# Performance work log

Measured on AMD Instinct MI355X. Metric: run time of the kernel, lower is better.

The kernel has to match this reference:

```python
import jax, jax.numpy as jnp
import numpy as np

N_EXPERTS = 8
TOP_K = 2


def setup_inputs() -> dict:
    key = jax.random.key(0)
    k1, k2, k3, k4 = jax.random.split(key, 4)
    B, S, D, E = 8, 4096, 1024, N_EXPERTS
    x = jax.random.normal(k1, (B, S, D), dtype=jnp.float32)
    gate_w = jax.random.normal(k2, (D, E), dtype=jnp.float32) * (1.0 / np.sqrt(D))
    expert_w = jax.random.normal(k3, (E, D, D), dtype=jnp.float32) * (1.0 / np.sqrt(D))
    expert_b = jax.random.normal(k4, (E, D), dtype=jnp.float32) * 0.01
    return {"x": x, "gate_w": gate_w, "expert_w": expert_w, "expert_b": expert_b}


def reference(x, gate_w, expert_w, expert_b):
    B, S, D = x.shape
    E = expert_w.shape[0]
    xt = x.reshape(-1, D)                       # [T, D], T = B*S
    T = xt.shape[0]
    gate_logits = xt @ gate_w                   # [T, E]
    weights, selected = jax.lax.top_k(gate_logits, TOP_K)   # [T, K]
    weights = jax.nn.softmax(weights.astype(jnp.float32), axis=1).astype(x.dtype)
    # Per-token combine weights over experts (top-k indices are distinct -> scatter-add is exact)
    combine = jnp.zeros((T, E), dtype=x.dtype).at[jnp.arange(T)[:, None], selected].add(weights)  # [T, E]
    out = jnp.zeros_like(xt)
    for e in range(E):  # fixed small expert count, mirrors the module's expert loop
        out = out + combine[:, e:e + 1] * (xt @ expert_w[e] + expert_b[e])
    return out.reshape(x.shape)
```

## Files before the change

### kernel.cpp

```cpp
#include <hip/hip_runtime.h>
#include <hip/hip_bf16.h>


typedef __attribute__((ext_vector_type(8))) short short8_t;
typedef __attribute__((ext_vector_type(4))) float f32x4_t;

#define GLOAD_LDS16(g, l)                                                                     \
  __builtin_amdgcn_global_load_lds((const __attribute__((address_space(1))) unsigned int*)(g), \
                                   (__attribute__((address_space(3))) unsigned int*)(l), 16, 0, 0)

__device__ __forceinline__ unsigned short f2bf(float f) {
  union { __hip_bfloat16 h; unsigned short u; } c;
  c.h = __float2bfloat16(f);
  return c.u;
}

__global__ __launch_bounds__(256) void gate_kernel(
    const float* __restrict__ x, const float* __restrict__ gw,
    unsigned short* __restrict__ xb,
    int* __restrict__ tok_e, float* __restrict__ tok_w)
{
  int wid = threadIdx.x >> 6, lane = threadIdx.x & 63;
  int t0 = (blockIdx.x << 4) + (wid << 2);
  const float4* g4 = (const float4*)gw;
  float lg[4][8] = {};
  #pragma unroll
  for (int c = 0; c < 4; ++c) {
    int d4 = (c << 6) + lane;
    float4 ga[4], gb[4];
    #pragma unroll
    for (int j = 0; j < 4; ++j) {
      int d = (d4 << 2) + j;
      ga[j] = g4[d << 1];
      gb[j] = g4[(d << 1) + 1];
    }
    #pragma unroll
    for (int t = 0; t < 4; ++t) {
      const float4* x4 = (const float4*)(x + ((size_t)(t0 + t) << 10));
      float4 v = x4[d4];
      unsigned long long pk = (unsigned long long)f2bf(v.x)
                            | ((unsigned long long)f2bf(v.y) << 16)
                            | ((unsigned long long)f2bf(v.z) << 32)
                            | ((unsigned long long)f2bf(v.w) << 48);
      ((unsigned long long*)(xb + ((size_t)(t0 + t) << 10)))[d4] = pk;
      float xs[4] = {v.x, v.y, v.z, v.w};
      #pragma unroll
      for (int j = 0; j < 4; ++j) {
        lg[t][0] += xs[j]*ga[j].x; lg[t][1] += xs[j]*ga[j].y;
        lg[t][2] += xs[j]*ga[j].z; lg[t][3] += xs[j]*ga[j].w;
        lg[t][4] += xs[j]*gb[j].x; lg[t][5] += xs[j]*gb[j].y;
        lg[t][6] += xs[j]*gb[j].z; lg[t][7] += xs[j]*gb[j].w;
      }
    }
  }
  #pragma unroll
  for (int t = 0; t < 4; ++t)
    #pragma unroll
    for (int e = 0; e < 8; ++e) {
      float v = lg[t][e];
      #pragma unroll
      for (int s = 32; s > 0; s >>= 1) v += __shfl_xor(v, s, 64);
      lg[t][e] = v;
    }
  if (lane < 4) {
    int t = t0 + lane;
    float m0 = lg[lane][0], m1 = -3.4e38f; int e0 = 0, e1 = 0;
    #pragma unroll
    for (int e = 1; e < 8; ++e) {
      float v = lg[lane][e];
      if (v > m0) { m1 = m0; e1 = e0; m0 = v; e0 = e; }
      else if (v > m1) { m1 = v; e1 = e; }
    }
    float p1 = 1.0f / (1.0f + expf(m0 - m1));
    float p0 = 1.0f - p1;
    int i0 = t << 1;
    tok_e[i0]   = e0; tok_w[i0]   = p0;
    tok_e[i0+1] = e1; tok_w[i0+1] = p1;
  }
}

__global__ __launch_bounds__(256) void hist_kernel(
    const int* __restrict__ tok_e, int* __restrict__ tok_r, int* __restrict__ chunkhist)
{
  __shared__ int lh[8];
  if (threadIdx.x < 8) lh[threadIdx.x] = 0;
  __syncthreads();
  int i = (blockIdx.x << 8) + threadIdx.x;
  int e = tok_e[i];
  tok_r[i] = atomicAdd(&lh[e], 1);
  __syncthreads();
  if (threadIdx.x < 8) chunkhist[(blockIdx.x << 3) + threadIdx.x] = lh[threadIdx.x];
}

__global__ __launch_bounds__(512) void scan_kernel(
    const int* __restrict__ chunkhist, int* __restrict__ base, int* __restrict__ ctrl)
{
  __shared__ int h[2048];
  __shared__ int bx[2048];
  __shared__ int tot[8], eoff[8];
  for (int i = threadIdx.x; i < 2048; i += 512) h[i] = chunkhist[i];
  __syncthreads();
  int wid = threadIdx.x >> 6, lane = threadIdx.x & 63;
  int running = 0;
  #pragma unroll
  for (int b = 0; b < 4; ++b) {
    int c = (b << 6) + lane;
    int orig = h[(c << 3) + wid];
    int v = orig;
    #pragma unroll
    for (int s = 1; s < 64; s <<= 1) {
      int u = __shfl_up(v, s, 64);
      if (lane >= s) v += u;
    }
    bx[(c << 3) + wid] = running + v - orig;
    running += __shfl(v, 63, 64);
  }
  if (lane == 0) tot[wid] = running;
  __syncthreads();
  if (threadIdx.x == 0) {
    int off = 0, boff = 0;
    #pragma unroll
    for (int e = 0; e < 8; ++e) {
      ctrl[e] = tot[e];
      ctrl[8 + e] = off; eoff[e] = off; off += tot[e];
      ctrl[16 + e] = boff; boff += (tot[e] + 127) >> 7;
    }
    ctrl[24] = boff;
  }
  __syncthreads();
  for (int i = threadIdx.x; i < 2048; i += 512) base[i] = bx[i] + eoff[i & 7];
}

__global__ __launch_bounds__(256) void scatter_kernel(
    const int* __restrict__ tok_e, const int* __restrict__ tok_r, const float* __restrict__ tok_w,
    const int* __restrict__ base, int* __restrict__ slot_token, float* __restrict__ slot_w,
    int* __restrict__ tok_slot)
{
  int i = (blockIdx.x << 8) + threadIdx.x;
  int e = tok_e[i];
  int slot = base[((i >> 8) << 3) + e] + tok_r[i];
  slot_token[slot] = i >> 1;
  slot_w[slot] = tok_w[i];
  tok_slot[i] = slot;
}

__global__ __launch_bounds__(256) void wconv_kernel(const float* __restrict__ w,
                                                    unsigned short* __restrict__ wt)
{
  __shared__ float tile[32][33];
  const float* we = w + ((size_t)blockIdx.z << 20);
  unsigned short* wte = wt + ((size_t)blockIdx.z << 20);
  int k0 = blockIdx.x << 5, n0 = blockIdx.y << 5;
  for (int i = threadIdx.x; i < 1024; i += 256) {
    int k = i >> 5, n = i & 31;
    tile[k][n] = we[(size_t)(k0 + k) * 1024 + n0 + n];
  }
  __syncthreads();
  for (int i = threadIdx.x; i < 1024; i += 256) {
    int n = i >> 5, k = i & 31;
    wte[(size_t)(n0 + n) * 1024 + k0 + k] = f2bf(tile[k][n]);
  }
}

__global__ __launch_bounds__(256, 3) void moe_gemm(
    const unsigned short* __restrict__ xb, const unsigned short* __restrict__ wt,
    const float* __restrict__ bias, const int* __restrict__ ctrl,
    const int* __restrict__ slot_token, const float* __restrict__ slot_w,
    float* __restrict__ ybuf, float* __restrict__ out, int total_slots, int use_ybuf)
{
  __shared__ unsigned short Alds[3 * 128 * 32];
  __shared__ unsigned short Blds[3 * 128 * 32];
  __shared__ int   tokid[128];
  __shared__ float wrow[128];

  int d = blockIdx.x;
  int s_ = d >> 3, xcd = d & 7;
  int by = ((s_ >> 3) << 3) | xcd;
  int bx = s_ & 7;
  if (by >= ctrl[24]) return;
  int e = 0;
  #pragma unroll
  for (int i = 1; i < 8; ++i) if (by >= ctrl[16 + i]) e = i;
  int mblk = by - ctrl[16 + e];
  int cnt  = ctrl[e];
  int slot0 = ctrl[8 + e] + (mblk << 7);
  int rows_valid = cnt - (mblk << 7); if (rows_valid > 128) rows_valid = 128;

  int tid = threadIdx.x;
  if (tid < 128) {
    int s = slot0 + tid; if (s > total_slots - 1) s = total_slots - 1;
    tokid[tid] = slot_token[s];
    wrow[tid]  = slot_w[s];
  }
  __syncthreads();

  int lane = tid & 63, w = tid >> 6;
  int wr = w >> 1, wc = w & 1;
  int l15 = lane & 15, hk = lane >> 4;
  int bn0 = bx << 7;
  const unsigned short* wte = wt + ((size_t)e << 20);

  int c0 = tid, c1 = tid + 256;
  int r0 = c0 >> 2, k0 = (c0 & 3) ^ ((r0 >> 1) & 3);
  int r1 = c1 >> 2, k1 = (c1 & 3) ^ ((r1 >> 1) & 3);
  const unsigned short* gA0 = xb + ((size_t)tokid[r0] << 10) + (k0 << 3);
  const unsigned short* gA1 = xb + ((size_t)tokid[r1] << 10) + (k1 << 3);
  const unsigned short* gB0 = wte + ((size_t)(bn0 + r0) << 10) + (k0 << 3);
  const unsigned short* gB1 = wte + ((size_t)(bn0 + r1) << 10) + (k1 << 3);
  int lo0 = (w << 6) << 3;
  int lo1 = ((w << 6) + 256) << 3;

  f32x4_t acc[4][4] = {};

#define STAGE(NB, KO)                                                         \
  GLOAD_LDS16(gA0 + (KO), &Alds[(NB) * 4096 + lo0]);                          \
  GLOAD_LDS16(gA1 + (KO), &Alds[(NB) * 4096 + lo1]);                          \
  GLOAD_LDS16(gB0 + (KO), &Blds[(NB) * 4096 + lo0]);                          \
  GLOAD_LDS16(gB1 + (KO), &Blds[(NB) * 4096 + lo1]);

#define COMPUTE(BUF)                                                          \
  { short8_t aF[4], bF[4];                                                    \
    _Pragma("unroll") for (int m = 0; m < 4; ++m) {                           \
      int ar = (wr << 6) + (m << 4) + l15;                                    \
      aF[m] = *(const short8_t*)&Alds[(BUF) * 4096 + (ar << 5) + ((hk ^ ((ar >> 1) & 3)) << 3)]; } \
    _Pragma("unroll") for (int n = 0; n < 4; ++n) {                           \
      int br = (wc << 6) + (n << 4) + l15;                                    \
      bF[n] = *(const short8_t*)&Blds[(BUF) * 4096 + (br << 5) + ((hk ^ ((br >> 1) & 3)) << 3)]; } \
    __builtin_amdgcn_s_setprio(1);                                            \
    _Pragma("unroll") for (int m = 0; m < 4; ++m)                             \
    _Pragma("unroll") for (int n = 0; n < 4; ++n)                             \
      acc[m][n] = __builtin_amdgcn_mfma_f32_16x16x32_bf16(aF[m], bF[n], acc[m][n], 0, 0, 0); \
    __builtin_amdgcn_s_setprio(0); }

#define VM4 asm volatile("s_waitcnt vmcnt(4)" ::: "memory");
#define BARR __builtin_amdgcn_s_barrier();

  STAGE(0, 0)
  STAGE(1, 32)
  VM4
  BARR
  for (int i = 0; i < 10; ++i) {
    int t = i * 3;
    STAGE(2, (t + 2) << 5)
    COMPUTE(0)
    VM4
    BARR
    STAGE(0, (t + 3) << 5)
    COMPUTE(1)
    VM4
    BARR
    STAGE(1, (t + 4) << 5)
    COMPUTE(2)
    VM4
    BARR
  }
  COMPUTE(0)
  asm volatile("s_waitcnt vmcnt(0)" ::: "memory");
  BARR
  COMPUTE(1)
#undef STAGE
#undef COMPUTE
#undef VM4
#undef BARR

  const float* be = bias + (e << 10);
  float bv[4];
  #pragma unroll
  for (int nf = 0; nf < 4; ++nf) bv[nf] = be[bn0 + (wc << 6) + (nf << 4) + l15];
  #pragma unroll
  for (int mf = 0; mf < 4; ++mf) {
    int rbase = (wr << 6) + (mf << 4) + (hk << 2);
    #pragma unroll
    for (int r = 0; r < 4; ++r) {
      int row = rbase + r;
      if (row < rows_valid) {
        float wv = wrow[row];
        if (use_ybuf) {
          size_t obase = ((size_t)(slot0 + row) << 10);
          #pragma unroll
          for (int nf = 0; nf < 4; ++nf) {
            int dout = bn0 + (wc << 6) + (nf << 4) + l15;
            ybuf[obase + dout] = wv * (acc[mf][nf][r] + bv[nf]);
          }
        } else {
          size_t obase = ((size_t)tokid[row] << 10);
          #pragma unroll
          for (int nf = 0; nf < 4; ++nf) {
            int dout = bn0 + (wc << 6) + (nf << 4) + l15;
            atomicAdd(&out[obase + dout], wv * (acc[mf][nf][r] + bv[nf]));
          }
        }
      }
    }
  }
}

__global__ __launch_bounds__(256) void combine_kernel(
    const float* __restrict__ ybuf, const int* __restrict__ tok_slot, float* __restrict__ out)
{
  int t = blockIdx.x;
  int s0 = tok_slot[t << 1], s1 = tok_slot[(t << 1) + 1];
  const float4* y0 = (const float4*)(ybuf + ((size_t)s0 << 10));
  const float4* y1 = (const float4*)(ybuf + ((size_t)s1 << 10));
  float4 a = y0[threadIdx.x], b = y1[threadIdx.x];
  float4 r; r.x = a.x + b.x; r.y = a.y + b.y; r.z = a.z + b.z; r.w = a.w + b.w;
  ((float4*)(out + ((size_t)t << 10)))[threadIdx.x] = r;
}

extern "C" void kernel_launch(void* const* d_in, const int* in_sizes, int n_in,
                              void* d_out, int out_size, void* d_ws, size_t ws_size,
                              hipStream_t stream) {
  (void)n_in;
  const float* x  = (const float*)d_in[0];
  const float* gw = (const float*)d_in[1];
  const float* ew = (const float*)d_in[2];
  const float* eb = (const float*)d_in[3];
  int T  = in_sizes[0] >> 10;
  int T2 = T << 1;

  char* wsb = (char*)d_ws;
  unsigned short* xb = (unsigned short*)wsb;
  size_t off = (size_t)T * 1024 * 2;
  unsigned short* wt = (unsigned short*)(wsb + off);
  off += (size_t)8 * 1024 * 1024 * 2;
  int* ctrl = (int*)(wsb + off); off += 256;
  int* tok_e = (int*)(wsb + off); off += (size_t)T2 * 4;
  int* tok_r = (int*)(wsb + off); off += (size_t)T2 * 4;
  float* tok_w = (float*)(wsb + off); off += (size_t)T2 * 4;
  int* slot_token = (int*)(wsb + off); off += (size_t)T2 * 4;
  float* slot_w = (float*)(wsb + off); off += (size_t)T2 * 4;
  int* tok_slot = (int*)(wsb + off); off += (size_t)T2 * 4;
  int* chunkhist = (int*)(wsb + off); off += 2048 * 4;
  int* base = (int*)(wsb + off); off += 2048 * 4;
  float* ybuf = (float*)(wsb + off);
  size_t need = off + (size_t)T2 * 1024 * 4;
  int use_ybuf = (ws_size >= need) ? 1 : 0;

  float* out = (float*)d_out;

  if (!use_ybuf)
    hipMemsetAsync(d_out, 0, (size_t)out_size * sizeof(float), stream);
  gate_kernel<<<T / 16, 256, 0, stream>>>(x, gw, xb, tok_e, tok_w);
  wconv_kernel<<<dim3(32, 32, 8), 256, 0, stream>>>(ew, wt);
  hist_kernel<<<T2 / 256, 256, 0, stream>>>(tok_e, tok_r, chunkhist);
  scan_kernel<<<1, 512, 0, stream>>>(chunkhist, base, ctrl);
  scatter_kernel<<<T2 / 256, 256, 0, stream>>>(tok_e, tok_r, tok_w, base,
                                               slot_token, slot_w, tok_slot);
  moe_gemm<<<4160, 256, 0, stream>>>(xb, wt, eb, ctrl, slot_token, slot_w,
                                     ybuf, out, T2, use_ybuf);
  if (use_ybuf)
    combine_kernel<<<T, 256, 0, stream>>>(ybuf, tok_slot, out);
}
```

Baseline: 365.1 us.

## Enlarge MoE GEMM tiles to 256x256 with 8 waves and phased pipelining

The grouped expert GEMM moves from 128x128 tiles with 4 waves and a triple-buffered K=32 pipeline to 256x256 tiles with 8 waves (2x4 layout), K=64 steps split into two halves, and double buffering. Loads and compute are interleaved in four phases per step, with finer-grained barriers and waitcnts. Expert blocks are now padded to 256 rows, and the grid shrinks to 1056 blocks. The goal is more arithmetic per byte loaded into LDS and fewer global loads. The costs are more padding waste per expert, larger LDS and register use that lowers occupancy, and fewer blocks to spread across CUs.

```diff
diff --git a/kernel.cpp b/kernel.cpp
--- a/kernel.cpp
+++ b/kernel.cpp
@@ -123,7 +123,7 @@
     for (int e = 0; e < 8; ++e) {
       ctrl[e] = tot[e];
       ctrl[8 + e] = off; eoff[e] = off; off += tot[e];
-      ctrl[16 + e] = boff; boff += (tot[e] + 127) >> 7;
+      ctrl[16 + e] = boff; boff += (tot[e] + 255) >> 8;
     }
     ctrl[24] = boff;
   }
@@ -162,32 +162,31 @@
   }
 }
 
-__global__ __launch_bounds__(256, 3) void moe_gemm(
+__global__ __launch_bounds__(512, 2) void moe_gemm(
     const unsigned short* __restrict__ xb, const unsigned short* __restrict__ wt,
     const float* __restrict__ bias, const int* __restrict__ ctrl,
     const int* __restrict__ slot_token, const float* __restrict__ slot_w,
     float* __restrict__ ybuf, float* __restrict__ out, int total_slots, int use_ybuf)
 {
-  __shared__ unsigned short Alds[3 * 128 * 32];
-  __shared__ unsigned short Blds[3 * 128 * 32];
-  __shared__ int   tokid[128];
-  __shared__ float wrow[128];
+  __shared__ unsigned short Alds[2 * 2 * 256 * 32];
+  __shared__ unsigned short Blds[2 * 2 * 256 * 32];
+  __shared__ int   tokid[256];
+  __shared__ float wrow[256];
 
   int d = blockIdx.x;
-  int s_ = d >> 3, xcd = d & 7;
-  int by = ((s_ >> 3) << 3) | xcd;
-  int bx = s_ & 7;
+  int xcd = d & 7, nb = (d >> 3) & 3, gbase = d >> 5;
+  int by = (gbase << 3) | xcd;
   if (by >= ctrl[24]) return;
   int e = 0;
   #pragma unroll
   for (int i = 1; i < 8; ++i) if (by >= ctrl[16 + i]) e = i;
   int mblk = by - ctrl[16 + e];
   int cnt  = ctrl[e];
-  int slot0 = ctrl[8 + e] + (mblk << 7);
-  int rows_valid = cnt - (mblk << 7); if (rows_valid > 128) rows_valid = 128;
+  int slot0 = ctrl[8 + e] + (mblk << 8);
+  int rows_valid = cnt - (mblk << 8); if (rows_valid > 256) rows_valid = 256;
 
   int tid = threadIdx.x;
-  if (tid < 128) {
+  if (tid < 256) {
     int s = slot0 + tid; if (s > total_slots - 1) s = total_slots - 1;
     tokid[tid] = slot_token[s];
     wrow[tid]  = slot_w[s];
@@ -195,81 +194,99 @@
   __syncthreads();
 
   int lane = tid & 63, w = tid >> 6;
-  int wr = w >> 1, wc = w & 1;
+  int wm = w >> 2, wn = w & 3;
   int l15 = lane & 15, hk = lane >> 4;
-  int bn0 = bx << 7;
+  int bn0 = nb << 8;
   const unsigned short* wte = wt + ((size_t)e << 20);
 
-  int c0 = tid, c1 = tid + 256;
-  int r0 = c0 >> 2, k0 = (c0 & 3) ^ ((r0 >> 1) & 3);
-  int r1 = c1 >> 2, k1 = (c1 & 3) ^ ((r1 >> 1) & 3);
-  const unsigned short* gA0 = xb + ((size_t)tokid[r0] << 10) + (k0 << 3);
-  const unsigned short* gA1 = xb + ((size_t)tokid[r1] << 10) + (k1 << 3);
-  const unsigned short* gB0 = wte + ((size_t)(bn0 + r0) << 10) + (k0 << 3);
-  const unsigned short* gB1 = wte + ((size_t)(bn0 + r1) << 10) + (k1 << 3);
-  int lo0 = (w << 6) << 3;
-  int lo1 = ((w << 6) + 256) << 3;
-
-  f32x4_t acc[4][4] = {};
-
-#define STAGE(NB, KO)                                                         \
-  GLOAD_LDS16(gA0 + (KO), &Alds[(NB) * 4096 + lo0]);                          \
-  GLOAD_LDS16(gA1 + (KO), &Alds[(NB) * 4096 + lo1]);                          \
-  GLOAD_LDS16(gB0 + (KO), &Blds[(NB) * 4096 + lo0]);                          \
-  GLOAD_LDS16(gB1 + (KO), &Blds[(NB) * 4096 + lo1]);
-
-#define COMPUTE(BUF)                                                          \
-  { short8_t aF[4], bF[4];                                                    \
-    _Pragma("unroll") for (int m = 0; m < 4; ++m) {                           \
-      int ar = (wr << 6) + (m << 4) + l15;                                    \
-      aF[m] = *(const short8_t*)&Alds[(BUF) * 4096 + (ar << 5) + ((hk ^ ((ar >> 1) & 3)) << 3)]; } \
-    _Pragma("unroll") for (int n = 0; n < 4; ++n) {                           \
-      int br = (wc << 6) + (n << 4) + l15;                                    \
-      bF[n] = *(const short8_t*)&Blds[(BUF) * 4096 + (br << 5) + ((hk ^ ((br >> 1) & 3)) << 3)]; } \
-    __builtin_amdgcn_s_setprio(1);                                            \
-    _Pragma("unroll") for (int m = 0; m < 4; ++m)                             \
-    _Pragma("unroll") for (int n = 0; n < 4; ++n)                             \
-      acc[m][n] = __builtin_amdgcn_mfma_f32_16x16x32_bf16(aF[m], bF[n], acc[m][n], 0, 0, 0); \
-    __builtin_amdgcn_s_setprio(0); }
-
-#define VM4 asm volatile("s_waitcnt vmcnt(4)" ::: "memory");
+  int rr = tid >> 2;
+  int kswz = (tid & 3) ^ ((tid >> 3) & 3);
+  const unsigned short* gA0 = xb + ((size_t)tokid[rr] << 10) + (kswz << 3);
+  const unsigned short* gA1 = xb + ((size_t)tokid[128 + rr] << 10) + (kswz << 3);
+  const unsigned short* gB0 = wte + ((size_t)(bn0 + rr) << 10) + (kswz << 3);
+  const unsigned short* gB1 = wte + ((size_t)(bn0 + 128 + rr) << 10) + (kswz << 3);
+
+  f32x4_t acc[8][4] = {};
+  short8_t aF[8], bFa[2], bFb[2];
+
+#define STG_A(BUF, KH, T)                                                               \
+  GLOAD_LDS16(gA0 + ((T) << 6) + ((KH) << 5), &Alds[(BUF) + ((KH) << 13) + (w << 9)]);  \
+  GLOAD_LDS16(gA1 + ((T) << 6) + ((KH) << 5), &Alds[(BUF) + ((KH) << 13) + 4096 + (w << 9)]);
+#define STG_B(BUF, KH, T)                                                               \
+  GLOAD_LDS16(gB0 + ((T) << 6) + ((KH) << 5), &Blds[(BUF) + ((KH) << 13) + (w << 9)]);  \
+  GLOAD_LDS16(gB1 + ((T) << 6) + ((KH) << 5), &Blds[(BUF) + ((KH) << 13) + 4096 + (w << 9)]);
+
+#define RD_AF(BUF, KH)                                                                  \
+  _Pragma("unroll") for (int mf = 0; mf < 8; ++mf) {                                    \
+    int ar = (wm << 7) + (mf << 4) + l15;                                               \
+    aF[mf] = *(const short8_t*)&Alds[(BUF) + ((KH) << 13) + (ar << 5) + ((hk ^ ((ar >> 1) & 3)) << 3)]; }
+#define RD_BF(DST, BUF, KH, NH)                                                         \
+  _Pragma("unroll") for (int i = 0; i < 2; ++i) {                                       \
+    int br = (wn << 6) + ((((NH) << 1) + i) << 4) + l15;                                \
+    DST[i] = *(const short8_t*)&Blds[(BUF) + ((KH) << 13) + (br << 5) + ((hk ^ ((br >> 1) & 3)) << 3)]; }
+
+#define MM(NH, BF)                                                                      \
+  __builtin_amdgcn_s_setprio(1);                                                        \
+  _Pragma("unroll") for (int mf = 0; mf < 8; ++mf)                                      \
+  _Pragma("unroll") for (int i = 0; i < 2; ++i)                                         \
+    acc[mf][((NH) << 1) + i] = __builtin_amdgcn_mfma_f32_16x16x32_bf16(                 \
+        aF[mf], BF[i], acc[mf][((NH) << 1) + i], 0, 0, 0);                              \
+  __builtin_amdgcn_s_setprio(0);
+
+#define PH_SYNC                                                                         \
+  __builtin_amdgcn_s_barrier();                                                         \
+  asm volatile("s_waitcnt lgkmcnt(0)" ::: "memory");                                    \
+  __builtin_amdgcn_sched_barrier(0);
 #define BARR __builtin_amdgcn_s_barrier();
 
-  STAGE(0, 0)
-  STAGE(1, 32)
-  VM4
+  STG_A(0, 0, 0) STG_B(0, 0, 0) STG_A(0, 1, 0) STG_B(0, 1, 0)
+  asm volatile("s_waitcnt vmcnt(4)" ::: "memory");
+  STG_A(16384, 0, 1) STG_B(16384, 0, 1) STG_A(16384, 1, 1)
+  asm volatile("s_waitcnt vmcnt(6)" ::: "memory");
   BARR
-  for (int i = 0; i < 10; ++i) {
-    int t = i * 3;
-    STAGE(2, (t + 2) << 5)
-    COMPUTE(0)
-    VM4
+
+  int cur = 0;
+  for (int t = 0; t < 16; ++t) {
+    int nxt = cur ^ 16384;
+    RD_AF(cur, 0) RD_BF(bFa, cur, 0, 0)
+    if (t < 15) { STG_B(nxt, 1, t + 1) }
+    PH_SYNC
+    MM(0, bFa)
     BARR
-    STAGE(0, (t + 3) << 5)
-    COMPUTE(1)
-    VM4
+    RD_BF(bFb, cur, 0, 1)
+    if (t < 14) { STG_A(cur, 0, t + 2) }
+    PH_SYNC
+    MM(1, bFb)
     BARR
-    STAGE(1, (t + 4) << 5)
-    COMPUTE(2)
-    VM4
+    RD_AF(cur, 1) RD_BF(bFa, cur, 1, 0)
+    if (t < 14) { STG_B(cur, 0, t + 2) }
+    PH_SYNC
+    MM(0, bFa)
     BARR
-  }
-  COMPUTE(0)
-  asm volatile("s_waitcnt vmcnt(0)" ::: "memory");
-  BARR
-  COMPUTE(1)
-#undef STAGE
-#undef COMPUTE
-#undef VM4
+    RD_BF(bFb, cur, 1, 1)
+    if (t < 14) { STG_A(cur, 1, t + 2) }
+    if (t < 14) { asm volatile("s_waitcnt vmcnt(6)" ::: "memory"); }
+    else if (t == 14) { asm volatile("s_waitcnt vmcnt(0)" ::: "memory"); }
+    PH_SYNC
+    MM(1, bFb)
+    BARR
+    cur = nxt;
+  }
+#undef STG_A
+#undef STG_B
+#undef RD_AF
+#undef RD_BF
+#undef MM
+#undef PH_SYNC
 #undef BARR
 
   const float* be = bias + (e << 10);
   float bv[4];
   #pragma unroll
-  for (int nf = 0; nf < 4; ++nf) bv[nf] = be[bn0 + (wc << 6) + (nf << 4) + l15];
-  #pragma unroll
-  for (int mf = 0; mf < 4; ++mf) {
-    int rbase = (wr << 6) + (mf << 4) + (hk << 2);
+  for (int nf = 0; nf < 4; ++nf) bv[nf] = be[bn0 + (wn << 6) + (nf << 4) + l15];
+  #pragma unroll
+  for (int mf = 0; mf < 8; ++mf) {
+    int rbase = (wm << 7) + (mf << 4) + (hk << 2);
     #pragma unroll
     for (int r = 0; r < 4; ++r) {
       int row = rbase + r;
@@ -279,14 +296,14 @@
           size_t obase = ((size_t)(slot0 + row) << 10);
           #pragma unroll
           for (int nf = 0; nf < 4; ++nf) {
-            int dout = bn0 + (wc << 6) + (nf << 4) + l15;
+            int dout = bn0 + (wn << 6) + (nf << 4) + l15;
             ybuf[obase + dout] = wv * (acc[mf][nf][r] + bv[nf]);
           }
         } else {
           size_t obase = ((size_t)tokid[row] << 10);
           #pragma unroll
           for (int nf = 0; nf < 4; ++nf) {
-            int dout = bn0 + (wc << 6) + (nf << 4) + l15;
+            int dout = bn0 + (wn << 6) + (nf << 4) + l15;
             atomicAdd(&out[obase + dout], wv * (acc[mf][nf][r] + bv[nf]));
           }
         }
@@ -346,7 +363,7 @@
   scan_kernel<<<1, 512, 0, stream>>>(chunkhist, base, ctrl);
   scatter_kernel<<<T2 / 256, 256, 0, stream>>>(tok_e, tok_r, tok_w, base,
                                                slot_token, slot_w, tok_slot);
-  moe_gemm<<<4160, 256, 0, stream>>>(xb, wt, eb, ctrl, slot_token, slot_w,
+  moe_gemm<<<1056, 512, 0, stream>>>(xb, wt, eb, ctrl, slot_token, slot_w,
                                      ybuf, out, T2, use_ybuf);
   if (use_ybuf)
     combine_kernel<<<T, 256, 0, stream>>>(ybuf, tok_slot, out);
```

After: 423.5 us. 16.0% more time.

## Widen MoE GEMM tile to 128x256 and store bf16 partials indexed by token

Applied to the files above, without the earlier changes.

The grouped expert GEMM tile grows from 128x128 to 128x256. Each wave now holds a 4x8 MFMA accumulator block, the B staging buffer doubles, and the grid is halved, which raises arithmetic intensity and cuts how often the gathered A rows are reloaded. Per-slot partial outputs are written in bf16 to a buffer indexed by token and k-slot rather than by slot, so the combine kernel no longer needs the tok_slot indirection and moves half the bytes. The costs are lower occupancy (launch bounds 2 instead of 3), higher register pressure, and extra rounding of the partial sums to bf16.

```diff
diff --git a/kernel.cpp b/kernel.cpp
--- a/kernel.cpp
+++ b/kernel.cpp
@@ -4,6 +4,7 @@
 
 typedef __attribute__((ext_vector_type(8))) short short8_t;
 typedef __attribute__((ext_vector_type(4))) float f32x4_t;
+typedef __attribute__((ext_vector_type(4))) unsigned short us4_t;
 
 #define GLOAD_LDS16(g, l)                                                                     \
   __builtin_amdgcn_global_load_lds((const __attribute__((address_space(1))) unsigned int*)(g), \
@@ -13,6 +14,11 @@
   union { __hip_bfloat16 h; unsigned short u; } c;
   c.h = __float2bfloat16(f);
   return c.u;
+}
+__device__ __forceinline__ float bf2f(unsigned short u) {
+  union { unsigned int i; float f; } c;
+  c.i = ((unsigned int)u) << 16;
+  return c.f;
 }
 
 __global__ __launch_bounds__(256) void gate_kernel(
@@ -133,15 +139,13 @@
 
 __global__ __launch_bounds__(256) void scatter_kernel(
     const int* __restrict__ tok_e, const int* __restrict__ tok_r, const float* __restrict__ tok_w,
-    const int* __restrict__ base, int* __restrict__ slot_token, float* __restrict__ slot_w,
-    int* __restrict__ tok_slot)
+    const int* __restrict__ base, int* __restrict__ slot_token, float* __restrict__ slot_w)
 {
   int i = (blockIdx.x << 8) + threadIdx.x;
   int e = tok_e[i];
   int slot = base[((i >> 8) << 3) + e] + tok_r[i];
-  slot_token[slot] = i >> 1;
+  slot_token[slot] = (i >> 1) | ((i & 1) << 16);
   slot_w[slot] = tok_w[i];
-  tok_slot[i] = slot;
 }
 
 __global__ __launch_bounds__(256) void wconv_kernel(const float* __restrict__ w,
@@ -162,21 +166,21 @@
   }
 }
 
-__global__ __launch_bounds__(256, 3) void moe_gemm(
+__global__ __launch_bounds__(256, 2) void moe_gemm(
     const unsigned short* __restrict__ xb, const unsigned short* __restrict__ wt,
     const float* __restrict__ bias, const int* __restrict__ ctrl,
     const int* __restrict__ slot_token, const float* __restrict__ slot_w,
-    float* __restrict__ ybuf, float* __restrict__ out, int total_slots, int use_ybuf)
+    unsigned short* __restrict__ part, float* __restrict__ out, int total_slots, int use_part)
 {
   __shared__ unsigned short Alds[3 * 128 * 32];
-  __shared__ unsigned short Blds[3 * 128 * 32];
+  __shared__ unsigned short Blds[3 * 256 * 32];
   __shared__ int   tokid[128];
+  __shared__ int   kslot[128];
   __shared__ float wrow[128];
 
   int d = blockIdx.x;
-  int s_ = d >> 3, xcd = d & 7;
-  int by = ((s_ >> 3) << 3) | xcd;
-  int bx = s_ & 7;
+  int xcd = d & 7, nb = (d >> 3) & 3, gbase = d >> 5;
+  int by = (gbase << 3) | xcd;
   if (by >= ctrl[24]) return;
   int e = 0;
   #pragma unroll
@@ -189,69 +193,73 @@
   int tid = threadIdx.x;
   if (tid < 128) {
     int s = slot0 + tid; if (s > total_slots - 1) s = total_slots - 1;
-    tokid[tid] = slot_token[s];
+    int v = slot_token[s];
+    tokid[tid] = v & 0xFFFF;
+    kslot[tid] = v >> 16;
     wrow[tid]  = slot_w[s];
   }
   __syncthreads();
 
   int lane = tid & 63, w = tid >> 6;
-  int wr = w >> 1, wc = w & 1;
+  int wm = w >> 1, wn = w & 1;
   int l15 = lane & 15, hk = lane >> 4;
-  int bn0 = bx << 7;
+  int bn0 = nb << 8;
   const unsigned short* wte = wt + ((size_t)e << 20);
 
-  int c0 = tid, c1 = tid + 256;
-  int r0 = c0 >> 2, k0 = (c0 & 3) ^ ((r0 >> 1) & 3);
-  int r1 = c1 >> 2, k1 = (c1 & 3) ^ ((r1 >> 1) & 3);
-  const unsigned short* gA0 = xb + ((size_t)tokid[r0] << 10) + (k0 << 3);
-  const unsigned short* gA1 = xb + ((size_t)tokid[r1] << 10) + (k1 << 3);
-  const unsigned short* gB0 = wte + ((size_t)(bn0 + r0) << 10) + (k0 << 3);
-  const unsigned short* gB1 = wte + ((size_t)(bn0 + r1) << 10) + (k1 << 3);
-  int lo0 = (w << 6) << 3;
-  int lo1 = ((w << 6) + 256) << 3;
-
-  f32x4_t acc[4][4] = {};
+  int rr = tid >> 2;
+  int kswz = (tid & 3) ^ ((tid >> 3) & 3);
+  const unsigned short* gA0 = xb + ((size_t)tokid[rr] << 10) + (kswz << 3);
+  const unsigned short* gA1 = xb + ((size_t)tokid[64 + rr] << 10) + (kswz << 3);
+  const unsigned short* gB0 = wte + ((size_t)(bn0 + rr) << 10) + (kswz << 3);
+  const unsigned short* gB1 = wte + ((size_t)(bn0 + 64 + rr) << 10) + (kswz << 3);
+  const unsigned short* gB2 = wte + ((size_t)(bn0 + 128 + rr) << 10) + (kswz << 3);
+  const unsigned short* gB3 = wte + ((size_t)(bn0 + 192 + rr) << 10) + (kswz << 3);
+  int wbase = w << 9;
+
+  f32x4_t acc[4][8] = {};
 
 #define STAGE(NB, KO)                                                         \
-  GLOAD_LDS16(gA0 + (KO), &Alds[(NB) * 4096 + lo0]);                          \
-  GLOAD_LDS16(gA1 + (KO), &Alds[(NB) * 4096 + lo1]);                          \
-  GLOAD_LDS16(gB0 + (KO), &Blds[(NB) * 4096 + lo0]);                          \
-  GLOAD_LDS16(gB1 + (KO), &Blds[(NB) * 4096 + lo1]);
+  GLOAD_LDS16(gA0 + (KO), &Alds[(NB) * 4096 + wbase]);                        \
+  GLOAD_LDS16(gA1 + (KO), &Alds[(NB) * 4096 + 2048 + wbase]);                 \
+  GLOAD_LDS16(gB0 + (KO), &Blds[(NB) * 8192 + wbase]);                        \
+  GLOAD_LDS16(gB1 + (KO), &Blds[(NB) * 8192 + 2048 + wbase]);                 \
+  GLOAD_LDS16(gB2 + (KO), &Blds[(NB) * 8192 + 4096 + wbase]);                 \
+  GLOAD_LDS16(gB3 + (KO), &Blds[(NB) * 8192 + 6144 + wbase]);
 
 #define COMPUTE(BUF)                                                          \
-  { short8_t aF[4], bF[4];                                                    \
+  { short8_t aF[4], bF[8];                                                    \
     _Pragma("unroll") for (int m = 0; m < 4; ++m) {                           \
-      int ar = (wr << 6) + (m << 4) + l15;                                    \
+      int ar = (wm << 6) + (m << 4) + l15;                                    \
       aF[m] = *(const short8_t*)&Alds[(BUF) * 4096 + (ar << 5) + ((hk ^ ((ar >> 1) & 3)) << 3)]; } \
-    _Pragma("unroll") for (int n = 0; n < 4; ++n) {                           \
-      int br = (wc << 6) + (n << 4) + l15;                                    \
-      bF[n] = *(const short8_t*)&Blds[(BUF) * 4096 + (br << 5) + ((hk ^ ((br >> 1) & 3)) << 3)]; } \
+    _Pragma("unroll") for (int n = 0; n < 8; ++n) {                           \
+      int br = (wn << 7) + (n << 4) + l15;                                    \
+      bF[n] = *(const short8_t*)&Blds[(BUF) * 8192 + (br << 5) + ((hk ^ ((br >> 1) & 3)) << 3)]; } \
     __builtin_amdgcn_s_setprio(1);                                            \
     _Pragma("unroll") for (int m = 0; m < 4; ++m)                             \
-    _Pragma("unroll") for (int n = 0; n < 4; ++n)                             \
+    _Pragma("unroll") for (int n = 0; n < 8; ++n)                             \
       acc[m][n] = __builtin_amdgcn_mfma_f32_16x16x32_bf16(aF[m], bF[n], acc[m][n], 0, 0, 0); \
     __builtin_amdgcn_s_setprio(0); }
 
-#define VM4 asm volatile("s_waitcnt vmcnt(4)" ::: "memory");
+#define VM6 asm volatile("s_waitcnt vmcnt(6)" ::: "memory");
 #define BARR __builtin_amdgcn_s_barrier();
 
   STAGE(0, 0)
   STAGE(1, 32)
-  VM4
+  VM6
   BARR
   for (int i = 0; i < 10; ++i) {
     int t = i * 3;
     STAGE(2, (t + 2) << 5)
     COMPUTE(0)
-    VM4
+    VM6
     BARR
     STAGE(0, (t + 3) << 5)
     COMPUTE(1)
-    VM4
+    VM6
     BARR
     STAGE(1, (t + 4) << 5)
     COMPUTE(2)
-    VM4
+    VM6
     BARR
   }
   COMPUTE(0)
@@ -260,33 +268,33 @@
   COMPUTE(1)
 #undef STAGE
 #undef COMPUTE
-#undef VM4
+#undef VM6
 #undef BARR
 
   const float* be = bias + (e << 10);
-  float bv[4];
-  #pragma unroll
-  for (int nf = 0; nf < 4; ++nf) bv[nf] = be[bn0 + (wc << 6) + (nf << 4) + l15];
+  float bv[8];
+  #pragma unroll
+  for (int nf = 0; nf < 8; ++nf) bv[nf] = be[bn0 + (wn << 7) + (nf << 4) + l15];
   #pragma unroll
   for (int mf = 0; mf < 4; ++mf) {
-    int rbase = (wr << 6) + (mf << 4) + (hk << 2);
+    int rbase = (wm << 6) + (mf << 4) + (hk << 2);
     #pragma unroll
     for (int r = 0; r < 4; ++r) {
       int row = rbase + r;
       if (row < rows_valid) {
         float wv = wrow[row];
-        if (use_ybuf) {
-          size_t obase = ((size_t)(slot0 + row) << 10);
+        if (use_part) {
+          size_t obase = ((size_t)((tokid[row] << 1) | kslot[row]) << 10);
           #pragma unroll
-          for (int nf = 0; nf < 4; ++nf) {
-            int dout = bn0 + (wc << 6) + (nf << 4) + l15;
-            ybuf[obase + dout] = wv * (acc[mf][nf][r] + bv[nf]);
+          for (int nf = 0; nf < 8; ++nf) {
+            int dout = bn0 + (wn << 7) + (nf << 4) + l15;
+            part[obase + dout] = f2bf(wv * (acc[mf][nf][r] + bv[nf]));
           }
         } else {
           size_t obase = ((size_t)tokid[row] << 10);
           #pragma unroll
-          for (int nf = 0; nf < 4; ++nf) {
-            int dout = bn0 + (wc << 6) + (nf << 4) + l15;
+          for (int nf = 0; nf < 8; ++nf) {
+            int dout = bn0 + (wn << 7) + (nf << 4) + l15;
             atomicAdd(&out[obase + dout], wv * (acc[mf][nf][r] + bv[nf]));
           }
         }
@@ -296,15 +304,18 @@
 }
 
 __global__ __launch_bounds__(256) void combine_kernel(
-    const float* __restrict__ ybuf, const int* __restrict__ tok_slot, float* __restrict__ out)
-{
-  int t = blockIdx.x;
-  int s0 = tok_slot[t << 1], s1 = tok_slot[(t << 1) + 1];
-  const float4* y0 = (const float4*)(ybuf + ((size_t)s0 << 10));
-  const float4* y1 = (const float4*)(ybuf + ((size_t)s1 << 10));
-  float4 a = y0[threadIdx.x], b = y1[threadIdx.x];
-  float4 r; r.x = a.x + b.x; r.y = a.y + b.y; r.z = a.z + b.z; r.w = a.w + b.w;
-  ((float4*)(out + ((size_t)t << 10)))[threadIdx.x] = r;
+    const unsigned short* __restrict__ part, float* __restrict__ out)
+{
+  int t = blockIdx.x, i = threadIdx.x;
+  const us4_t* p0 = (const us4_t*)(part + ((size_t)(t << 1) << 10));
+  const us4_t* p1 = (const us4_t*)(part + ((size_t)((t << 1) | 1) << 10));
+  us4_t a = p0[i], b = p1[i];
+  float4 r;
+  r.x = bf2f(a.x) + bf2f(b.x);
+  r.y = bf2f(a.y) + bf2f(b.y);
+  r.z = bf2f(a.z) + bf2f(b.z);
+  r.w = bf2f(a.w) + bf2f(b.w);
+  ((float4*)(out + ((size_t)t << 10)))[i] = r;
 }
 
 extern "C" void kernel_launch(void* const* d_in, const int* in_sizes, int n_in,
@@ -329,25 +340,24 @@
   float* tok_w = (float*)(wsb + off); off += (size_t)T2 * 4;
   int* slot_token = (int*)(wsb + off); off += (size_t)T2 * 4;
   float* slot_w = (float*)(wsb + off); off += (size_t)T2 * 4;
-  int* tok_slot = (int*)(wsb + off); off += (size_t)T2 * 4;
   int* chunkhist = (int*)(wsb + off); off += 2048 * 4;
   int* base = (int*)(wsb + off); off += 2048 * 4;
-  float* ybuf = (float*)(wsb + off);
-  size_t need = off + (size_t)T2 * 1024 * 4;
-  int use_ybuf = (ws_size >= need) ? 1 : 0;
+  unsigned short* part = (unsigned short*)(wsb + off);
+  size_t need = off + (size_t)T2 * 1024 * 2;
+  int use_part = (ws_size >= need) ? 1 : 0;
 
   float* out = (float*)d_out;
 
-  if (!use_ybuf)
+  if (!use_part)
     hipMemsetAsync(d_out, 0, (size_t)out_size * sizeof(float), stream);
   gate_kernel<<<T / 16, 256, 0, stream>>>(x, gw, xb, tok_e, tok_w);
   wconv_kernel<<<dim3(32, 32, 8), 256, 0, stream>>>(ew, wt);
   hist_kernel<<<T2 / 256, 256, 0, stream>>>(tok_e, tok_r, chunkhist);
   scan_kernel<<<1, 512, 0, stream>>>(chunkhist, base, ctrl);
   scatter_kernel<<<T2 / 256, 256, 0, stream>>>(tok_e, tok_r, tok_w, base,
-                                               slot_token, slot_w, tok_slot);
-  moe_gemm<<<4160, 256, 0, stream>>>(xb, wt, eb, ctrl, slot_token, slot_w,
-                                     ybuf, out, T2, use_ybuf);
-  if (use_ybuf)
-    combine_kernel<<<T, 256, 0, stream>>>(ybuf, tok_slot, out);
-}
+                                               slot_token, slot_w);
+  moe_gemm<<<2080, 256, 0, stream>>>(xb, wt, eb, ctrl, slot_token, slot_w,
+                                     part, out, T2, use_part);
+  if (use_part)
+    combine_kernel<<<T, 256, 0, stream>>>(part, out);
+}
```

Result: faster. 307.9 us (-15.7%).
